# Optimization experiments

Hardware: AMD Instinct MI355X
Metric: run time of the kernel (lower is better)

## Reference

```python
import jax, jax.numpy as jnp
import numpy as np

N_HEAD, D_MODEL, D_HEAD = 16, 1024, 64
LN_EPS = 1e-5


def setup_inputs() -> dict:
    key = jax.random.key(0)
    ks = jax.random.split(key, 12)
    S, B = 1024, 8
    nd = N_HEAD * D_HEAD
    sc = 0.02
    return {
        "hidden_states": jax.random.normal(ks[0], (S, B, D_MODEL), jnp.float32),
        "rel_pos_emb": jax.random.normal(ks[1], (S, D_MODEL), jnp.float32),
        "encoder_hidden_states": jax.random.normal(ks[2], (S, B, D_MODEL), jnp.float32),
        "W_q": jax.random.normal(ks[3], (D_MODEL, nd), jnp.float32) * sc,
        "W_kv": jax.random.normal(ks[4], (D_MODEL, 2 * nd), jnp.float32) * sc,
        "W_r": jax.random.normal(ks[5], (D_MODEL, nd), jnp.float32) * sc,
        "W_o": jax.random.normal(ks[6], (nd, D_MODEL), jnp.float32) * sc,
        "r_w_bias": jax.random.normal(ks[7], (N_HEAD, D_HEAD), jnp.float32) * sc,
        "r_r_bias": jax.random.normal(ks[8], (N_HEAD, D_HEAD), jnp.float32) * sc,
        "ln_gamma": jnp.ones((D_MODEL,), jnp.float32),
        "ln_beta": jnp.zeros((D_MODEL,), jnp.float32),
    }


def _rel_shift(x):
    # x: (qlen, rlen, bsz, n_head) -- Transformer-XL relative shift trick
    q, r, b, n = x.shape
    zero_pad = jnp.zeros((q, 1, b, n), x.dtype)
    x_padded = jnp.concatenate([zero_pad, x], axis=1).reshape(r + 1, q, b, n)
    return x_padded[1:].reshape(q, r, b, n)


def _layer_norm(x, gamma, beta):
    mu = jnp.mean(x, axis=-1, keepdims=True)
    var = jnp.mean(jnp.square(x - mu), axis=-1, keepdims=True)
    return (x - mu) * jax.lax.rsqrt(var + LN_EPS) * gamma + beta


def reference(hidden_states, rel_pos_emb, encoder_hidden_states,
              W_q, W_kv, W_r, W_o, r_w_bias, r_r_bias, ln_gamma, ln_beta):
    qlen, bsz, _ = hidden_states.shape
    rlen = rel_pos_emb.shape[0]
    # post-lnorm path (pre_lnorm=False), no mems, no mask, eval (dropout off)
    mem_heads = encoder_hidden_states @ W_kv            # (klen, b, 2*n*d)
    w_head_q = hidden_states @ W_q                      # (qlen, b, n*d)
    r_head_k = rel_pos_emb @ W_r                        # (rlen, n*d)
    w_head_k, w_head_v = jnp.split(mem_heads, 2, axis=-1)
    klen = w_head_k.shape[0]

    w_head_q = w_head_q.reshape(qlen, bsz, N_HEAD, D_HEAD)
    w_head_k = w_head_k.reshape(klen, bsz, N_HEAD, D_HEAD)
    w_head_v = w_head_v.reshape(klen, bsz, N_HEAD, D_HEAD)
    r_head_k = r_head_k.reshape(rlen, N_HEAD, D_HEAD)

    scale = 1.0 / (D_HEAD ** 0.5)
    AC = jnp.einsum('ibnd,jbnd->ijbn', w_head_q + r_w_bias, w_head_k)
    BD = jnp.einsum('ibnd,jnd->ijbn', w_head_q + r_r_bias, r_head_k)
    BD = _rel_shift(BD)
    attn_score = (AC + BD) * scale                      # (q, k, b, n)

    attn_prob = jax.nn.softmax(attn_score, axis=1)
    attn_vec = jnp.einsum('ijbn,jbnd->ibnd', attn_prob, w_head_v)
    attn_vec = attn_vec.reshape(qlen, bsz, N_HEAD * D_HEAD)
    attn_out = attn_vec @ W_o
    return _layer_norm(hidden_states + attn_out, ln_gamma, ln_beta)
```

## Files before the change

kernel.cpp:

```cpp
#include <hip/hip_runtime.h>
#include <stdint.h>

constexpr int SEQ = 1024;
constexpr int BSZ = 8;
constexpr int NHEAD = 16;
constexpr int DHEAD = 64;
constexpr int DMODEL = 1024;

using u16 = unsigned short;
using bf16x8 = __attribute__((ext_vector_type(8))) short;
using f32x4 = __attribute__((ext_vector_type(4))) float;

__device__ __forceinline__ float bf2f(u16 u) {
  union { unsigned int i; float f; } c; c.i = ((unsigned int)u) << 16; return c.f;
}
__device__ __forceinline__ u16 f2bf(float f) {
  union { float f; unsigned int i; } c; c.f = f;
  unsigned int x = c.i;
  return (u16)((x + 0x7FFFu + ((x >> 16) & 1u)) >> 16);
}
__device__ __forceinline__ unsigned cvtpk(float a, float b) {
  unsigned r; asm("v_cvt_pk_bf16_f32 %0, %1, %2" : "=v"(r) : "v"(a), "v"(b)); return r;
}
__device__ __forceinline__ float exp2v(float x) {
  float r; asm("v_exp_f32 %0, %1" : "=v"(r) : "v"(x)); return r;
}
__device__ __forceinline__ void gload16(const void* g, void* l) {
  __builtin_amdgcn_global_load_lds((const __attribute__((address_space(1))) void*)g,
                                   (__attribute__((address_space(3))) void*)l, 16, 0, 0);
}
__device__ __forceinline__ bf16x8 cvt8(const float* src) {
  f32x4 a = *(const f32x4*)src;
  f32x4 b = *(const f32x4*)(src + 4);
  union { unsigned u[4]; bf16x8 v; } o;
  o.u[0] = cvtpk(a[0], a[1]); o.u[1] = cvtpk(a[2], a[3]);
  o.u[2] = cvtpk(b[0], b[1]); o.u[3] = cvtpk(b[2], b[3]);
  return o.v;
}
__device__ __forceinline__ bf16x8 rd8(const u16* base, int row, int col) {
  return *(const bf16x8*)((const char*)base + (((row * 64 + col) * 2) ^ ((row & 7) << 4)));
}
__device__ __forceinline__ bf16x8 rd8_128(const u16* base, int row, int col) {
  return *(const bf16x8*)((const char*)base + (((row * 128 + col) * 2) ^ ((row & 7) << 4)));
}
__device__ __forceinline__ void wr128(u16* base, int row, int col, u16 v) {
  *(u16*)((char*)base + (((row * 128 + col) * 2) ^ ((row & 7) << 4))) = v;
}

template <int A32, int C32>
__global__ __launch_bounds__(256, 2) void gemm_bt(
    const void* __restrict__ Ap, int lda,
    const u16* __restrict__ BT, int ldb,
    void* __restrict__ Cp, int ldc, int K) {
  __shared__ __align__(16) u16 As[128 * 64];
  __shared__ __align__(16) u16 Bs[128 * 64];
  const int t = threadIdx.x;
  const int lane = t & 63;
  const int w = t >> 6, wr = w >> 1, wc = w & 1;
  const int l15 = lane & 15, l4 = lane >> 4;
  const int row0 = blockIdx.y * 128, col0 = blockIdx.x * 128;
  f32x4 acc[4][4] = {};
  for (int k0 = 0; k0 < K; k0 += 64) {
#pragma unroll
    for (int q = 0; q < 4; q++) {
      int u = q * 256 + t;
      int r = u >> 3, c8 = u & 7;
      int sc8 = c8 ^ (r & 7);
      int ub = (q * 256 + (t & ~63)) * 8;
      gload16(BT + (size_t)(col0 + r) * ldb + k0 + sc8 * 8, Bs + ub);
      if (A32) {
        const float* src = (const float*)Ap + (size_t)(row0 + r) * lda + k0 + sc8 * 8;
        *(bf16x8*)(As + (size_t)u * 8) = cvt8(src);
      } else {
        gload16((const u16*)Ap + (size_t)(row0 + r) * lda + k0 + sc8 * 8, As + ub);
      }
    }
    __syncthreads();
#pragma unroll
    for (int kk = 0; kk < 2; kk++) {
      bf16x8 av[4], bv[4];
#pragma unroll
      for (int f = 0; f < 4; f++) {
        int kb = kk * 32 + l4 * 8;
        av[f] = rd8(As, wr * 64 + f * 16 + l15, kb);
        bv[f] = rd8(Bs, wc * 64 + f * 16 + l15, kb);
      }
#pragma unroll
      for (int fr = 0; fr < 4; fr++)
#pragma unroll
        for (int fc = 0; fc < 4; fc++)
          acc[fr][fc] = __builtin_amdgcn_mfma_f32_16x16x32_bf16(av[fr], bv[fc], acc[fr][fc], 0, 0, 0);
    }
    __syncthreads();
  }
#pragma unroll
  for (int fr = 0; fr < 4; fr++)
#pragma unroll
    for (int fc = 0; fc < 4; fc++) {
      int col = col0 + wc * 64 + fc * 16 + l15;
      int rw0 = row0 + wr * 64 + fr * 16 + l4 * 4;
      if (C32) {
#pragma unroll
        for (int r = 0; r < 4; r++)
          ((float*)Cp)[(size_t)(rw0 + r) * ldc + col] = acc[fr][fc][r];
      } else {
        unsigned p01 = cvtpk(acc[fr][fc][0], acc[fr][fc][1]);
        unsigned p23 = cvtpk(acc[fr][fc][2], acc[fr][fc][3]);
        u16* cb = (u16*)Cp;
        cb[(size_t)(rw0 + 0) * ldc + col] = (u16)p01;
        cb[(size_t)(rw0 + 1) * ldc + col] = (u16)(p01 >> 16);
        cb[(size_t)(rw0 + 2) * ldc + col] = (u16)p23;
        cb[(size_t)(rw0 + 3) * ldc + col] = (u16)(p23 >> 16);
      }
    }
}

__global__ void corr_kernel(const u16* __restrict__ Rh, const float* __restrict__ rwb,
                            const float* __restrict__ rrb, float* __restrict__ corrR) {
  const int m0 = blockIdx.x * 64, n = blockIdx.y;
  const int t = threadIdx.x, r = t >> 2, q = t & 3;
  float p = 0.f;
#pragma unroll
  for (int e = 0; e < 16; e++) {
    int d = q * 16 + e;
    p += (rrb[n * DHEAD + d] - rwb[n * DHEAD + d]) * bf2f(Rh[(size_t)(m0 + r) * DMODEL + n * DHEAD + d]);
  }
  p += __shfl_xor(p, 1, 4);
  p += __shfl_xor(p, 2, 4);
  if (q == 0) corrR[n * SEQ + m0 + r] = p;
}

__global__ __launch_bounds__(256, 3) void flash_fused(
    const u16* __restrict__ Qb, const u16* __restrict__ KVb,
    const u16* __restrict__ VT, const u16* __restrict__ Rh,
    const float* __restrict__ rwb, const float* __restrict__ corrR,
    u16* __restrict__ AV) {
  __shared__ __align__(16) char smem[49408];
  u16* Qs = (u16*)smem;
  u16* Ks = (u16*)(smem + 8320);
  u16* Vs = (u16*)(smem + 16512);
  u16* Rs = (u16*)(smem + 24704);
  u16* Df = (u16*)(smem + 32896);
  const int t = threadIdx.x;
  const int lane = t & 63;
  const int w = t >> 6;
  const int l15 = lane & 15, l4 = lane >> 4;
  const int bid = blockIdx.x;
  const int sw = (bid & 7) * 256 + (bid >> 3);
  const int i0 = (sw & 15) * 64;
  const int z = sw >> 4, b = z >> 4, n = z & 15;
  const float KSC = 0.18033688f;

#pragma unroll
  for (int p = 0; p < 3; p++) {
    int u = p * 256 + t;
    if (u < 520) {
      int r = u >> 3, c8 = u & 7;
      int sc8 = c8 ^ (r & 7);
      int rq = i0 + r; if (rq > SEQ - 1) rq = SEQ - 1;
      bf16x8 qv = *(const bf16x8*)(Qb + ((size_t)rq * BSZ + b) * DMODEL + n * DHEAD + sc8 * 8);
      f32x4 b0 = *(const f32x4*)(rwb + n * DHEAD + sc8 * 8);
      f32x4 b1 = *(const f32x4*)(rwb + n * DHEAD + sc8 * 8 + 4);
      union { unsigned u4[4]; bf16x8 v; } o;
      o.u4[0] = cvtpk(bf2f((u16)qv[0]) + b0[0], bf2f((u16)qv[1]) + b0[1]);
      o.u4[1] = cvtpk(bf2f((u16)qv[2]) + b0[2], bf2f((u16)qv[3]) + b0[3]);
      o.u4[2] = cvtpk(bf2f((u16)qv[4]) + b1[0], bf2f((u16)qv[5]) + b1[1]);
      o.u4[3] = cvtpk(bf2f((u16)qv[6]) + b1[2], bf2f((u16)qv[7]) + b1[3]);
      *(bf16x8*)(Qs + (size_t)u * 8) = o.v;
    }
  }
  const int baseP = (SEQ - 64) - i0;
  const float* corrn = corrR + n * SEQ;
#pragma unroll
  for (int q = 0; q < 2; q++) {
    int u = q * 256 + t;
    int r = u >> 3, c8 = u & 7;
    int sc8 = c8 ^ (r & 7);
    int ub = (q * 256 + (t & ~63)) * 8;
    gload16(Rh + (size_t)(baseP + r) * DMODEL + n * DHEAD + sc8 * 8, Rs + ub);
  }
  float cP[4];
#pragma unroll
  for (int fc = 0; fc < 4; fc++) cP[fc] = corrn[baseP + fc * 16 + l15];
  __syncthreads();
  {
    f32x4 dp[4] = {};
#pragma unroll
    for (int kk = 0; kk < 2; kk++) {
      int kb = kk * 32 + l4 * 8;
      bf16x8 aQ = rd8(Qs, w * 16 + l15, kb);
#pragma unroll
      for (int fc = 0; fc < 4; fc++)
        dp[fc] = __builtin_amdgcn_mfma_f32_16x16x32_bf16(aQ, rd8(Rs, fc * 16 + l15, kb), dp[fc], 0, 0, 0);
    }
#pragma unroll
    for (int r = 0; r < 4; r++) {
      int row = w * 16 + l4 * 4 + r;
      unsigned d01 = cvtpk(dp[0][r] + cP[0], dp[1][r] + cP[1]);
      unsigned d23 = cvtpk(dp[2][r] + cP[2], dp[3][r] + cP[3]);
      wr128(Df, row, 0 * 16 + l15, (u16)d01);
      wr128(Df, row, 1 * 16 + l15, (u16)(d01 >> 16));
      wr128(Df, row, 2 * 16 + l15, (u16)d23);
      wr128(Df, row, 3 * 16 + l15, (u16)(d23 >> 16));
    }
  }
  f32x4 O[4] = {};
  float M[4], Lp[4];
#pragma unroll
  for (int r = 0; r < 4; r++) { M[r] = -1e30f; Lp[r] = 0.f; }
  float spec = 0.f;

  for (int jj = 0; jj < 16; jj++) {
    const int j0 = jj * 64;
    const int dlt = j0 - i0;
    const int base2 = (dlt < 0) ? dlt + SEQ : dlt;
    const int qo2 = (dlt >= 0) ? 1 : 0;
    const int off = (jj & 1) << 6;
    __syncthreads();
#pragma unroll
    for (int q = 0; q < 2; q++) {
      int u = q * 256 + t;
      int r = u >> 3, c8 = u & 7;
      int sc8 = c8 ^ (r & 7);
      int ub = (q * 256 + (t & ~63)) * 8;
      gload16(KVb + ((size_t)(j0 + r) * BSZ + b) * (2 * DMODEL) + n * DHEAD + sc8 * 8, Ks + ub);
      gload16(VT + ((size_t)(b * NHEAD + n) * DHEAD + r) * SEQ + j0 + sc8 * 8, Vs + ub);
      gload16(Rh + (size_t)(base2 + r) * DMODEL + n * DHEAD + sc8 * 8, Rs + ub);
    }
    float cr[4];
#pragma unroll
    for (int fc = 0; fc < 4; fc++) cr[fc] = corrn[base2 + fc * 16 + l15];
    __syncthreads();
    f32x4 sacc[4] = {}, dnew[4] = {};
    __builtin_amdgcn_s_setprio(1);
#pragma unroll
    for (int kk = 0; kk < 2; kk++) {
      int kb = kk * 32 + l4 * 8;
      int qr0 = w * 16 + l15;
      bf16x8 aQ = rd8(Qs, qr0, kb);
      bf16x8 aD = rd8(Qs, qr0 + qo2, kb);
#pragma unroll
      for (int fc = 0; fc < 4; fc++) {
        int br = fc * 16 + l15;
        sacc[fc] = __builtin_amdgcn_mfma_f32_16x16x32_bf16(aQ, rd8(Ks, br, kb), sacc[fc], 0, 0, 0);
        dnew[fc] = __builtin_amdgcn_mfma_f32_16x16x32_bf16(aD, rd8(Rs, br, kb), dnew[fc], 0, 0, 0);
      }
    }
    __builtin_amdgcn_s_setprio(0);
    const int offn = off ^ 64;
#pragma unroll
    for (int r = 0; r < 4; r++) {
      int row = w * 16 + l4 * 4 + r;
      unsigned d01 = cvtpk(dnew[0][r] + cr[0], dnew[1][r] + cr[1]);
      unsigned d23 = cvtpk(dnew[2][r] + cr[2], dnew[3][r] + cr[3]);
      wr128(Df, row, offn + 0 * 16 + l15, (u16)d01);
      wr128(Df, row, offn + 1 * 16 + l15, (u16)(d01 >> 16));
      wr128(Df, row, offn + 2 * 16 + l15, (u16)d23);
      wr128(Df, row, offn + 3 * 16 + l15, (u16)(d23 >> 16));
    }
    float specnext = 0.f;
    if (w == 3)
      specnext = bf2f(*(const u16*)((const char*)Df + ((63 * 256) | ((((off + 63) * 2) ^ 0x70)))));
    const float fix = (dlt == 64) ? 0.f : spec;
#pragma unroll
    for (int r = 0; r < 4; r++) {
      const int lrow = w * 16 + l4 * 4 + r;
      const int rbase = lrow * 256;
      const int swz = (lrow & 7) << 4;
      float v2[4];
      if (dlt < 0) {
        const int K = off + 63 - lrow;
#pragma unroll
        for (int fc = 0; fc < 4; fc++) {
          int col = (fc * 16 + l15 + K) & 127;
          float bd = bf2f(*(const u16*)((const char*)Df + (rbase | ((col * 2) ^ swz))));
          v2[fc] = (sacc[fc][r] + bd) * KSC;
        }
      } else if (dlt == 0) {
#pragma unroll
        for (int fc = 0; fc < 4; fc++) {
          int dj = fc * 16 + l15 - lrow;
          int ul = (dj <= 0) ? dj + 63 : dj + 62;
          int col = (off + ul) & 127;
          float bd = bf2f(*(const u16*)((const char*)Df + (rbase | ((col * 2) ^ swz))));
          if (dj == 1) bd = 0.f;
          v2[fc] = (sacc[fc][r] + bd) * KSC;
        }
      } else {
        const int K = 62 - lrow;
#pragma unroll
        for (int fc = 0; fc < 4; fc++) {
          int ul = fc * 16 + l15 + K;
          int col = (off + ((ul < 0) ? 0 : ul)) & 127;
          float bd = bf2f(*(const u16*)((const char*)Df + (rbase | ((col * 2) ^ swz))));
          if (ul < 0) bd = fix;
          v2[fc] = (sacc[fc][r] + bd) * KSC;
        }
      }
      float tm = fmaxf(fmaxf(v2[0], v2[1]), fmaxf(v2[2], v2[3]));
      unsigned long long bal = __ballot(tm > M[r] + 11.5f);
      if ((bal >> (l4 * 16)) & 0xFFFFull) {
        for (int mk = 1; mk < 16; mk <<= 1) tm = fmaxf(tm, __shfl_xor(tm, mk, 16));
        float alpha = exp2v(M[r] - tm);
        Lp[r] *= alpha;
#pragma unroll
        for (int fd = 0; fd < 4; fd++) O[fd][r] *= alpha;
        M[r] = tm;
      }
      float e0 = exp2v(v2[0] - M[r]), e1 = exp2v(v2[1] - M[r]);
      float e2 = exp2v(v2[2] - M[r]), e3 = exp2v(v2[3] - M[r]);
      Lp[r] += (e0 + e1) + (e2 + e3);
      unsigned p01 = cvtpk(e0, e1), p23 = cvtpk(e2, e3);
      wr128(Df, lrow, off + 0 * 16 + l15, (u16)p01);
      wr128(Df, lrow, off + 1 * 16 + l15, (u16)(p01 >> 16));
      wr128(Df, lrow, off + 2 * 16 + l15, (u16)p23);
      wr128(Df, lrow, off + 3 * 16 + l15, (u16)(p23 >> 16));
    }
    spec = specnext;
    __builtin_amdgcn_s_setprio(1);
#pragma unroll
    for (int kk = 0; kk < 2; kk++) {
      int kb = kk * 32 + l4 * 8;
      bf16x8 a = rd8_128(Df, w * 16 + l15, off + kb);
#pragma unroll
      for (int fd = 0; fd < 4; fd++)
        O[fd] = __builtin_amdgcn_mfma_f32_16x16x32_bf16(a, rd8(Vs, fd * 16 + l15, kb), O[fd], 0, 0, 0);
    }
    __builtin_amdgcn_s_setprio(0);
  }
  float Lf[4];
#pragma unroll
  for (int r = 0; r < 4; r++) {
    float Lt = Lp[r];
    for (int mk = 1; mk < 16; mk <<= 1) Lt += __shfl_xor(Lt, mk, 16);
    Lf[r] = 1.f / Lt;
  }
#pragma unroll
  for (int fd = 0; fd < 4; fd++) {
    int d = fd * 16 + l15;
    int iq0 = i0 + w * 16 + l4 * 4;
    unsigned p01 = cvtpk(O[fd][0] * Lf[0], O[fd][1] * Lf[1]);
    unsigned p23 = cvtpk(O[fd][2] * Lf[2], O[fd][3] * Lf[3]);
    AV[((size_t)(iq0 + 0) * BSZ + b) * DMODEL + n * DHEAD + d] = (u16)p01;
    AV[((size_t)(iq0 + 1) * BSZ + b) * DMODEL + n * DHEAD + d] = (u16)(p01 >> 16);
    AV[((size_t)(iq0 + 2) * BSZ + b) * DMODEL + n * DHEAD + d] = (u16)p23;
    AV[((size_t)(iq0 + 3) * BSZ + b) * DMODEL + n * DHEAD + d] = (u16)(p23 >> 16);
  }
}

__global__ void wtrans(const float* __restrict__ in, u16* __restrict__ out, int R, int C) {
  __shared__ unsigned int lds[64][65];
  const int t = threadIdx.x;
  const int c0 = blockIdx.x * 64, r0 = blockIdx.y * 64;
#pragma unroll
  for (int p = 0; p < 2; p++) {
    int u = p * 256 + t;
    int r = u >> 3, c8 = u & 7;
    const float* src = in + (size_t)(r0 + r) * C + c0 + c8 * 8;
    f32x4 v0 = *(const f32x4*)src;
    f32x4 v1 = *(const f32x4*)(src + 4);
    unsigned q0 = cvtpk(v0[0], v0[1]), q1 = cvtpk(v0[2], v0[3]);
    unsigned q2 = cvtpk(v1[0], v1[1]), q3 = cvtpk(v1[2], v1[3]);
    lds[r][c8 * 8 + 0] = (u16)q0; lds[r][c8 * 8 + 1] = (u16)(q0 >> 16);
    lds[r][c8 * 8 + 2] = (u16)q1; lds[r][c8 * 8 + 3] = (u16)(q1 >> 16);
    lds[r][c8 * 8 + 4] = (u16)q2; lds[r][c8 * 8 + 5] = (u16)(q2 >> 16);
    lds[r][c8 * 8 + 6] = (u16)q3; lds[r][c8 * 8 + 7] = (u16)(q3 >> 16);
  }
  __syncthreads();
#pragma unroll
  for (int p = 0; p < 2; p++) {
    int u = p * 256 + t;
    int r = u >> 3, c8 = u & 7;
    bf16x8 v;
#pragma unroll
    for (int e = 0; e < 8; e++) v[e] = (short)lds[c8 * 8 + e][r];
    *(bf16x8*)(out + (size_t)(c0 + r) * R + r0 + c8 * 8) = v;
  }
}

__global__ void vtrans(const u16* __restrict__ KVb, u16* __restrict__ VT) {
  __shared__ unsigned int lds[64][65];
  const int t = threadIdx.x;
  const int s0 = blockIdx.x * 64, n = blockIdx.y, b = blockIdx.z;
#pragma unroll
  for (int p = 0; p < 2; p++) {
    int u = p * 256 + t;
    int r = u >> 3, c8 = u & 7;
    const u16* src = KVb + ((size_t)(s0 + r) * BSZ + b) * (2 * DMODEL) + DMODEL + n * DHEAD + c8 * 8;
    bf16x8 v = *(const bf16x8*)src;
#pragma unroll
    for (int e = 0; e < 8; e++) lds[r][c8 * 8 + e] = (u16)v[e];
  }
  __syncthreads();
#pragma unroll
  for (int p = 0; p < 2; p++) {
    int u = p * 256 + t;
    int r = u >> 3, c8 = u & 7;
    bf16x8 v;
#pragma unroll
    for (int e = 0; e < 8; e++) v[e] = (short)lds[c8 * 8 + e][r];
    *(bf16x8*)(VT + ((size_t)(b * NHEAD + n) * DHEAD + r) * SEQ + s0 + c8 * 8) = v;
  }
}

__global__ void ln_kernel(const float* __restrict__ hidden,
                          const float* __restrict__ gamma, const float* __restrict__ beta,
                          float* __restrict__ out) {
  __shared__ float wsum[4];
  __shared__ float wvar[4];
  const int row = blockIdx.x;
  const int t = threadIdx.x;
  f32x4 hv = *(const f32x4*)(hidden + (size_t)row * DMODEL + t * 4);
  f32x4 ov = *(const f32x4*)(out + (size_t)row * DMODEL + t * 4);
  float xs[4], sum = 0.f;
#pragma unroll
  for (int e = 0; e < 4; e++) { xs[e] = hv[e] + ov[e]; sum += xs[e]; }
  for (int mk = 1; mk < 64; mk <<= 1) sum += __shfl_xor(sum, mk, 64);
  if ((t & 63) == 0) wsum[t >> 6] = sum;
  __syncthreads();
  float mu = (wsum[0] + wsum[1] + wsum[2] + wsum[3]) * (1.f / DMODEL);
  float var = 0.f;
#pragma unroll
  for (int e = 0; e < 4; e++) { float d = xs[e] - mu; var += d * d; }
  for (int mk = 1; mk < 64; mk <<= 1) var += __shfl_xor(var, mk, 64);
  if ((t & 63) == 0) wvar[t >> 6] = var;
  __syncthreads();
  float rstd = rsqrtf((wvar[0] + wvar[1] + wvar[2] + wvar[3]) * (1.f / DMODEL) + 1e-5f);
  f32x4 res;
#pragma unroll
  for (int e = 0; e < 4; e++) {
    int c = t * 4 + e;
    res[e] = (xs[e] - mu) * rstd * gamma[c] + beta[c];
  }
  *(f32x4*)(out + (size_t)row * DMODEL + t * 4) = res;
}

extern "C" void kernel_launch(void* const* d_in, const int* in_sizes, int n_in,
                              void* d_out, int out_size, void* d_ws, size_t ws_size,
                              hipStream_t stream) {
  const float* hidden = (const float*)d_in[0];
  const float* relpos = (const float*)d_in[1];
  const float* enc    = (const float*)d_in[2];
  const float* W_q    = (const float*)d_in[3];
  const float* W_kv   = (const float*)d_in[4];
  const float* W_r    = (const float*)d_in[5];
  const float* W_o    = (const float*)d_in[6];
  const float* rwb    = (const float*)d_in[7];
  const float* rrb    = (const float*)d_in[8];
  const float* gamma  = (const float*)d_in[9];
  const float* beta   = (const float*)d_in[10];
  float* out = (float*)d_out;

  char* ws = (char*)d_ws;
  size_t off = 0;
  auto alloc = [&](size_t bytes) { char* p = ws + off; off += (bytes + 255) & ~(size_t)255; return p; };
  const size_t MB = 1024 * 1024;
  u16* WOT  = (u16*)alloc(2 * MB);
  u16* Qb   = (u16*)alloc(16 * MB);
  u16* KVb  = (u16*)alloc(32 * MB);
  u16* VT   = (u16*)alloc(16 * MB);
  u16* AV   = (u16*)alloc(16 * MB);
  u16* Rh   = (u16*)alloc(2 * MB);
  float* corrR = (float*)alloc(NHEAD * SEQ * 4);
  u16* WQT  = (u16*)alloc(2 * MB);
  u16* WKVT = (u16*)alloc(4 * MB);
  u16* WRT  = (u16*)alloc(2 * MB);
  (void)ws_size; (void)in_sizes; (void)n_in; (void)out_size;

  dim3 blk(256);
  wtrans<<<dim3(16, 16), blk, 0, stream>>>(W_q, WQT, 1024, 1024);
  wtrans<<<dim3(32, 16), blk, 0, stream>>>(W_kv, WKVT, 1024, 2048);
  wtrans<<<dim3(16, 16), blk, 0, stream>>>(W_r, WRT, 1024, 1024);
  wtrans<<<dim3(16, 16), blk, 0, stream>>>(W_o, WOT, 1024, 1024);

  gemm_bt<1, 0><<<dim3(8, 64), blk, 0, stream>>>(hidden, 1024, WQT, 1024, Qb, 1024, 1024);
  gemm_bt<1, 0><<<dim3(16, 64), blk, 0, stream>>>(enc, 1024, WKVT, 1024, KVb, 2048, 1024);
  gemm_bt<1, 0><<<dim3(8, 8), blk, 0, stream>>>(relpos, 1024, WRT, 1024, Rh, 1024, 1024);
  corr_kernel<<<dim3(16, NHEAD), blk, 0, stream>>>(Rh, rwb, rrb, corrR);
  vtrans<<<dim3(16, NHEAD, BSZ), blk, 0, stream>>>(KVb, VT);

  flash_fused<<<dim3(16 * BSZ * NHEAD), blk, 0, stream>>>(Qb, KVb, VT, Rh, rwb, corrR, AV);

  gemm_bt<0, 1><<<dim3(8, 64), blk, 0, stream>>>(AV, 1024, WOT, 1024, out, 1024, 1024);
  ln_kernel<<<dim3(8192), blk, 0, stream>>>(hidden, gamma, beta, out);
}
```

Before: 329.5 us.

## Load K, V, R operands straight from global memory instead of staging in LDS

The flash attention kernel no longer stages K, V and R tiles through shared memory with global_load_lds and barriers. Each wave now reads its MFMA B operands directly from global memory, and the Q fragments are hoisted into registers once. LDS use shrinks to the Q and Df buffers and launch bounds rise to 4 blocks per CU, aiming at higher occupancy and fewer barriers. The cost is redundant global or L2 traffic, because all four waves load the same K/V/R tiles, plus exposed load latency in the inner loop. The Df exchange still relies on wave-local ordering without the removed barriers.

```diff
diff --git a/kernel.cpp b/kernel.cpp
--- a/kernel.cpp
+++ b/kernel.cpp
@@ -13,11 +13,6 @@
 
 __device__ __forceinline__ float bf2f(u16 u) {
   union { unsigned int i; float f; } c; c.i = ((unsigned int)u) << 16; return c.f;
-}
-__device__ __forceinline__ u16 f2bf(float f) {
-  union { float f; unsigned int i; } c; c.f = f;
-  unsigned int x = c.i;
-  return (u16)((x + 0x7FFFu + ((x >> 16) & 1u)) >> 16);
 }
 __device__ __forceinline__ unsigned cvtpk(float a, float b) {
   unsigned r; asm("v_cvt_pk_bf16_f32 %0, %1, %2" : "=v"(r) : "v"(a), "v"(b)); return r;
@@ -130,17 +125,14 @@
   if (q == 0) corrR[n * SEQ + m0 + r] = p;
 }
 
-__global__ __launch_bounds__(256, 3) void flash_fused(
+__global__ __launch_bounds__(256, 4) void flash_fused(
     const u16* __restrict__ Qb, const u16* __restrict__ KVb,
     const u16* __restrict__ VT, const u16* __restrict__ Rh,
     const float* __restrict__ rwb, const float* __restrict__ corrR,
     u16* __restrict__ AV) {
-  __shared__ __align__(16) char smem[49408];
+  __shared__ __align__(16) char smem[24704];
   u16* Qs = (u16*)smem;
-  u16* Ks = (u16*)(smem + 8320);
-  u16* Vs = (u16*)(smem + 16512);
-  u16* Rs = (u16*)(smem + 24704);
-  u16* Df = (u16*)(smem + 32896);
+  u16* Df = (u16*)(smem + 8320);
   const int t = threadIdx.x;
   const int lane = t & 63;
   const int w = t >> 6;
@@ -169,29 +161,32 @@
       *(bf16x8*)(Qs + (size_t)u * 8) = o.v;
     }
   }
+  __syncthreads();
+  bf16x8 aQ[2], aD1[2];
+#pragma unroll
+  for (int kk = 0; kk < 2; kk++) {
+    int kb = kk * 32 + l4 * 8;
+    aQ[kk]  = rd8(Qs, w * 16 + l15, kb);
+    aD1[kk] = rd8(Qs, w * 16 + l15 + 1, kb);
+  }
+  const u16* Kbase = KVb + (size_t)b * (2 * DMODEL) + n * DHEAD;
+  const u16* Vbase = VT + ((size_t)(b * NHEAD + n) * DHEAD) * SEQ;
+  const float* corrn = corrR + n * SEQ;
+
   const int baseP = (SEQ - 64) - i0;
-  const float* corrn = corrR + n * SEQ;
-#pragma unroll
-  for (int q = 0; q < 2; q++) {
-    int u = q * 256 + t;
-    int r = u >> 3, c8 = u & 7;
-    int sc8 = c8 ^ (r & 7);
-    int ub = (q * 256 + (t & ~63)) * 8;
-    gload16(Rh + (size_t)(baseP + r) * DMODEL + n * DHEAD + sc8 * 8, Rs + ub);
-  }
-  float cP[4];
-#pragma unroll
-  for (int fc = 0; fc < 4; fc++) cP[fc] = corrn[baseP + fc * 16 + l15];
-  __syncthreads();
   {
+    float cP[4];
+#pragma unroll
+    for (int fc = 0; fc < 4; fc++) cP[fc] = corrn[baseP + fc * 16 + l15];
     f32x4 dp[4] = {};
 #pragma unroll
     for (int kk = 0; kk < 2; kk++) {
       int kb = kk * 32 + l4 * 8;
-      bf16x8 aQ = rd8(Qs, w * 16 + l15, kb);
-#pragma unroll
-      for (int fc = 0; fc < 4; fc++)
-        dp[fc] = __builtin_amdgcn_mfma_f32_16x16x32_bf16(aQ, rd8(Rs, fc * 16 + l15, kb), dp[fc], 0, 0, 0);
+#pragma unroll
+      for (int fc = 0; fc < 4; fc++) {
+        bf16x8 rB = *(const bf16x8*)(Rh + (size_t)(baseP + fc * 16 + l15) * DMODEL + n * DHEAD + kb);
+        dp[fc] = __builtin_amdgcn_mfma_f32_16x16x32_bf16(aQ[kk], rB, dp[fc], 0, 0, 0);
+      }
     }
 #pragma unroll
     for (int r = 0; r < 4; r++) {
@@ -216,34 +211,22 @@
     const int base2 = (dlt < 0) ? dlt + SEQ : dlt;
     const int qo2 = (dlt >= 0) ? 1 : 0;
     const int off = (jj & 1) << 6;
-    __syncthreads();
-#pragma unroll
-    for (int q = 0; q < 2; q++) {
-      int u = q * 256 + t;
-      int r = u >> 3, c8 = u & 7;
-      int sc8 = c8 ^ (r & 7);
-      int ub = (q * 256 + (t & ~63)) * 8;
-      gload16(KVb + ((size_t)(j0 + r) * BSZ + b) * (2 * DMODEL) + n * DHEAD + sc8 * 8, Ks + ub);
-      gload16(VT + ((size_t)(b * NHEAD + n) * DHEAD + r) * SEQ + j0 + sc8 * 8, Vs + ub);
-      gload16(Rh + (size_t)(base2 + r) * DMODEL + n * DHEAD + sc8 * 8, Rs + ub);
-    }
     float cr[4];
 #pragma unroll
     for (int fc = 0; fc < 4; fc++) cr[fc] = corrn[base2 + fc * 16 + l15];
-    __syncthreads();
     f32x4 sacc[4] = {}, dnew[4] = {};
     __builtin_amdgcn_s_setprio(1);
 #pragma unroll
     for (int kk = 0; kk < 2; kk++) {
       int kb = kk * 32 + l4 * 8;
-      int qr0 = w * 16 + l15;
-      bf16x8 aQ = rd8(Qs, qr0, kb);
-      bf16x8 aD = rd8(Qs, qr0 + qo2, kb);
+      bf16x8 aD = qo2 ? aD1[kk] : aQ[kk];
 #pragma unroll
       for (int fc = 0; fc < 4; fc++) {
         int br = fc * 16 + l15;
-        sacc[fc] = __builtin_amdgcn_mfma_f32_16x16x32_bf16(aQ, rd8(Ks, br, kb), sacc[fc], 0, 0, 0);
-        dnew[fc] = __builtin_amdgcn_mfma_f32_16x16x32_bf16(aD, rd8(Rs, br, kb), dnew[fc], 0, 0, 0);
+        bf16x8 kB = *(const bf16x8*)(Kbase + (size_t)(j0 + br) * (BSZ * 2 * DMODEL) + kb);
+        bf16x8 rB = *(const bf16x8*)(Rh + (size_t)(base2 + br) * DMODEL + n * DHEAD + kb);
+        sacc[fc] = __builtin_amdgcn_mfma_f32_16x16x32_bf16(aQ[kk], kB, sacc[fc], 0, 0, 0);
+        dnew[fc] = __builtin_amdgcn_mfma_f32_16x16x32_bf16(aD, rB, dnew[fc], 0, 0, 0);
       }
     }
     __builtin_amdgcn_s_setprio(0);
@@ -323,8 +306,10 @@
       int kb = kk * 32 + l4 * 8;
       bf16x8 a = rd8_128(Df, w * 16 + l15, off + kb);
 #pragma unroll
-      for (int fd = 0; fd < 4; fd++)
-        O[fd] = __builtin_amdgcn_mfma_f32_16x16x32_bf16(a, rd8(Vs, fd * 16 + l15, kb), O[fd], 0, 0, 0);
+      for (int fd = 0; fd < 4; fd++) {
+        bf16x8 vB = *(const bf16x8*)(Vbase + (size_t)(fd * 16 + l15) * SEQ + j0 + kb);
+        O[fd] = __builtin_amdgcn_mfma_f32_16x16x32_bf16(a, vB, O[fd], 0, 0, 0);
+      }
     }
     __builtin_amdgcn_s_setprio(0);
   }
```

After: 648.3 us. +96.7%, slower.
